# Performance work log

Measured on AMD Instinct MI355X. Metric: run time of the kernel, lower is better.

The kernel has to match this reference:

```python
import jax, jax.numpy as jnp
import numpy as np

X_SIZE = 300
H_SIZE = 128
N_CLASSES = 5
K = 3          # branching factor of the complete tree
LEVELS = 11    # tree depth (levels 0..10); N = (K**LEVELS - 1)//(K - 1) = 88573


def _build_tree():
    counts = K ** np.arange(LEVELS)
    n = int(counts.sum())
    level = np.repeat(np.arange(LEVELS), counts).astype(np.int32)
    idx = np.arange(n)
    parent = np.maximum((idx - 1) // K, 0).astype(np.int32)  # BFS numbering
    return n, parent, level


def setup_inputs() -> dict:
    key = jax.random.key(0)
    ks = jax.random.split(key, 8)
    n, parent, level = _build_tree()
    s = 0.05  # weight init scale
    return {
        "x": jax.random.normal(ks[0], (n, X_SIZE), jnp.float32),
        "mask": jax.random.randint(ks[1], (n,), 0, 2).astype(bool),
        "W_iou": jax.random.normal(ks[2], (X_SIZE, 3 * H_SIZE), jnp.float32) * s,
        "b_iou": jnp.zeros((3 * H_SIZE,), jnp.float32),
        "W_f": jax.random.normal(ks[3], (X_SIZE, H_SIZE), jnp.float32) * s,
        "b_f": jnp.zeros((H_SIZE,), jnp.float32),
        "U_iou": jax.random.normal(ks[4], (H_SIZE, 3 * H_SIZE), jnp.float32) * s,
        "U_f": jax.random.normal(ks[5], (H_SIZE, H_SIZE), jnp.float32) * s,
        "W_out": jax.random.normal(ks[6], (H_SIZE, N_CLASSES), jnp.float32) * s,
        "b_out": jnp.zeros((N_CLASSES,), jnp.float32),
        "parent": jnp.asarray(parent),
        "level": jnp.asarray(level),
        "n_levels": LEVELS,
    }


def reference(x, mask, W_iou, b_iou, W_f, b_f, U_iou, U_f, W_out, b_out,
              parent, level, n_levels):
    n = x.shape[0]
    h_size = U_f.shape[0]
    m = mask.astype(x.dtype)[:, None]                  # [N,1]
    embeds = x * m                                     # input_module = identity
    iou_in = (embeds @ W_iou + b_iou) * m              # [N,3H]
    f_in = (embeds @ W_f + b_f) * m                    # [N,H]

    h = jnp.zeros((n, h_size), x.dtype)
    c = jnp.zeros((n, h_size), x.dtype)
    par = parent[1:]                                   # edge child->parent, children are nodes 1..N-1

    # bottom-up topological propagation, one level at a time (child-sum cell)
    for lvl in range(n_levels - 1, -1, -1):
        h_ch = h[1:]                                   # children hidden states
        f = jax.nn.sigmoid(f_in[par] + h_ch @ U_f)     # per-edge forget gate
        h_sum = jax.ops.segment_sum(h_ch, par, num_segments=n)
        fc_sum = jax.ops.segment_sum(f * c[1:], par, num_segments=n)
        iou = iou_in + h_sum @ U_iou
        i, o, u = jnp.split(iou, 3, axis=-1)
        i, o, u = jax.nn.sigmoid(i), jax.nn.sigmoid(o), jnp.tanh(u)
        c_new = i * u + fc_sum
        h_new = o * jnp.tanh(c_new)
        at = (level == lvl)[:, None]
        h = jnp.where(at, h_new, h)
        c = jnp.where(at, c_new, c)

    return h @ W_out + b_out                           # output_module: Linear(H, 5)
```

## Files before the change

kernel.cpp:

```cpp
#include <hip/hip_runtime.h>
#include <hip/hip_bf16.h>
#include <math.h>

#define H 128
#define XS 300
#define NCLS 5
#define KPAD 320
#define NXCD 8

typedef __attribute__((ext_vector_type(8))) short short8;
typedef __attribute__((ext_vector_type(4))) float f32x4;

static __device__ inline unsigned short f2bf(float f) {
    __hip_bfloat16 h = __float2bfloat16(f);
    return *reinterpret_cast<unsigned short*>(&h);
}
static __device__ inline float bf2f(unsigned short u) {
    unsigned int x = ((unsigned int)u) << 16;
    return __builtin_bit_cast(float, x);
}
static __device__ inline float sigm(float v) { return 1.f / (1.f + __expf(-v)); }

__global__ void mask_conv_kernel(const void* __restrict__ mask_raw,
                                 float* __restrict__ m, int n) {
    const unsigned int* w = (const unsigned int*)mask_raw;
    bool is_bytes = false;
#pragma unroll
    for (int i = 0; i < 16; i++) is_bytes |= (w[i] > 1u);
    int idx = blockIdx.x * blockDim.x + threadIdx.x;
    if (idx >= n) return;
    float mv;
    if (is_bytes) mv = ((const unsigned char*)mask_raw)[idx] ? 1.f : 0.f;
    else          mv = ((const int*)mask_raw)[idx] ? 1.f : 0.f;
    m[idx] = mv;
}

__global__ void wconv_kernel(const float* __restrict__ W_iou,
                             const float* __restrict__ W_f,
                             unsigned short* __restrict__ Wb_t) {
    int c = blockIdx.x;
    int k = threadIdx.x;
    float v = 0.f;
    if (k < XS) v = (c < 384) ? W_iou[(size_t)k * 384 + c]
                              : W_f[(size_t)k * 128 + (c - 384)];
    Wb_t[(size_t)c * KPAD + k] = f2bf(v);
}

__global__ void uconv_kernel(const float* __restrict__ U_f,
                             const float* __restrict__ U_iou,
                             unsigned short* __restrict__ Uf_hi,
                             unsigned short* __restrict__ Uf_lo,
                             unsigned short* __restrict__ Uiou_hi,
                             unsigned short* __restrict__ Uiou_lo) {
    int c = blockIdx.x;
    int k = threadIdx.x;
    if (c < 128) {
        float v = U_f[(size_t)k * 128 + c];
        unsigned short hi = f2bf(v);
        Uf_hi[(size_t)c * 128 + k] = hi;
        Uf_lo[(size_t)c * 128 + k] = f2bf(v - bf2f(hi));
    } else {
        int cc = c - 128;
        float v = U_iou[(size_t)k * 384 + cc];
        unsigned short hi = f2bf(v);
        Uiou_hi[(size_t)cc * 128 + k] = hi;
        Uiou_lo[(size_t)cc * 128 + k] = f2bf(v - bf2f(hi));
    }
}

__global__ __launch_bounds__(256) void gemm_in_mfma(
    const float* __restrict__ x, const float* __restrict__ m,
    const unsigned short* __restrict__ Wb_t,
    const float* __restrict__ b_iou, const float* __restrict__ b_f,
    float* __restrict__ iou_in, float* __restrict__ f_in, int n)
{
    __shared__ __align__(16) unsigned short Asld[128][72];
    __shared__ __align__(16) unsigned short Bsld[128][72];

    int bid = blockIdx.x;
    int nwg = gridDim.x;
    int q = nwg / NXCD, r = nwg % NXCD;
    int xcd = bid % NXCD, slot = bid / NXCD;
    int nid = (xcd < r) ? (xcd * (q + 1) + slot)
                        : (r * (q + 1) + (xcd - r) * q + slot);
    int bn = nid & 3;
    int bm = nid >> 2;

    int t    = threadIdx.x;
    int lane = t & 63;
    int wid  = t >> 6;
    int wr = wid >> 1, wc = wid & 1;

    int r0 = bm * 128;
    int c0 = bn * 128;

    f32x4 acc[4][4];
#pragma unroll
    for (int i = 0; i < 4; i++)
#pragma unroll
        for (int j = 0; j < 4; j++) acc[i][j] = (f32x4)0.f;

    for (int k0 = 0; k0 < KPAD; k0 += 64) {
        {
            int rr = t >> 4;
            int kq = (t & 15) << 2;
            int kg = k0 + kq;
#pragma unroll
            for (int p = 0; p < 8; p++) {
                int row  = r0 + rr + p * 16;
                int rowc = row < n ? row : n - 1;
                float4 v;
                if (kg + 4 <= XS) v = *(const float4*)&x[(size_t)rowc * XS + kg];
                else              v = make_float4(0.f, 0.f, 0.f, 0.f);
                ushort4 b4;
                b4.x = f2bf(v.x); b4.y = f2bf(v.y);
                b4.z = f2bf(v.z); b4.w = f2bf(v.w);
                *(ushort4*)&Asld[rr + p * 16][kq] = b4;
            }
        }
        {
            int rr  = t >> 3;
            int kq8 = (t & 7) << 3;
#pragma unroll
            for (int p = 0; p < 4; p++) {
                int col = c0 + rr + p * 32;
                uint4 v = *(const uint4*)&Wb_t[(size_t)col * KPAD + k0 + kq8];
                *(uint4*)&Bsld[rr + p * 32][kq8] = v;
            }
        }
        __syncthreads();

#pragma unroll
        for (int ks = 0; ks < 2; ks++) {
            int kc = ks * 32 + (lane >> 4) * 8;
            short8 af[4], bf[4];
#pragma unroll
            for (int mi = 0; mi < 4; mi++)
                af[mi] = *(const short8*)&Asld[wr * 64 + mi * 16 + (lane & 15)][kc];
#pragma unroll
            for (int ni = 0; ni < 4; ni++)
                bf[ni] = *(const short8*)&Bsld[wc * 64 + ni * 16 + (lane & 15)][kc];
#pragma unroll
            for (int mi = 0; mi < 4; mi++)
#pragma unroll
                for (int ni = 0; ni < 4; ni++)
                    acc[mi][ni] = __builtin_amdgcn_mfma_f32_16x16x32_bf16(
                        af[mi], bf[ni], acc[mi][ni], 0, 0, 0);
        }
        __syncthreads();
    }

    const float* bias;
    float* outp;
    int ldw, colbase;
    if (bn < 3) { bias = b_iou; outp = iou_in; ldw = 384; colbase = bn * 128; }
    else        { bias = b_f;   outp = f_in;   ldw = 128; colbase = 0; }

    float bias_v[4];
#pragma unroll
    for (int ni = 0; ni < 4; ni++)
        bias_v[ni] = bias[colbase + wc * 64 + ni * 16 + (lane & 15)];

#pragma unroll
    for (int mi = 0; mi < 4; mi++) {
#pragma unroll
        for (int j = 0; j < 4; j++) {
            int row = r0 + wr * 64 + mi * 16 + (lane >> 4) * 4 + j;
            if (row >= n) continue;
            float mv = m[row];
#pragma unroll
            for (int ni = 0; ni < 4; ni++) {
                int col = colbase + wc * 64 + ni * 16 + (lane & 15);
                outp[(size_t)row * ldw + col] = mv * (acc[mi][ni][j] + bias_v[ni]);
            }
        }
    }
}

__global__ void leaf_kernel(const float* __restrict__ iou_in,
                            unsigned short* __restrict__ h_hi,
                            unsigned short* __restrict__ h_lo,
                            float* __restrict__ c,
                            int start, int count)
{
    int idx = blockIdx.x * blockDim.x + threadIdx.x;
    int total = count * 32;
    if (idx >= total) return;
    int v = start + (idx >> 5);
    int d = (idx & 31) * 4;
    const float* row = iou_in + (size_t)v * 384;
    float4 iv = *(const float4*)&row[d];
    float4 ov = *(const float4*)&row[128 + d];
    float4 uv = *(const float4*)&row[256 + d];
    float cv[4], hv[4];
    float ivv[4] = {iv.x, iv.y, iv.z, iv.w};
    float ovv[4] = {ov.x, ov.y, ov.z, ov.w};
    float uvv[4] = {uv.x, uv.y, uv.z, uv.w};
#pragma unroll
    for (int e = 0; e < 4; e++) {
        float ig = sigm(ivv[e]), og = sigm(ovv[e]), ug = tanhf(uvv[e]);
        cv[e] = ig * ug;
        hv[e] = og * tanhf(cv[e]);
    }
    *(float4*)&c[(size_t)v * H + d] = make_float4(cv[0], cv[1], cv[2], cv[3]);
    ushort4 hh, hl;
    unsigned short s;
    s = f2bf(hv[0]); hh.x = s; hl.x = f2bf(hv[0] - bf2f(s));
    s = f2bf(hv[1]); hh.y = s; hl.y = f2bf(hv[1] - bf2f(s));
    s = f2bf(hv[2]); hh.z = s; hl.z = f2bf(hv[2] - bf2f(s));
    s = f2bf(hv[3]); hh.w = s; hl.w = f2bf(hv[3] - bf2f(s));
    *(ushort4*)&h_hi[(size_t)v * H + d] = hh;
    *(ushort4*)&h_lo[(size_t)v * H + d] = hl;
}

__global__ __launch_bounds__(256) void level_gemm_f(
    const unsigned short* __restrict__ h_hi, const unsigned short* __restrict__ h_lo,
    const float* __restrict__ c, float* fbuf,
    const unsigned short* __restrict__ Uf_hi, const unsigned short* __restrict__ Uf_lo,
    int P0, int NP)
{
    __shared__ __align__(16) unsigned short Ah[64][136];
    __shared__ __align__(16) unsigned short Al[64][136];

    int C0 = 3 * P0 + 1;
    int M3 = 3 * NP;
    int r0 = blockIdx.x * 64;
    int t = threadIdx.x;

    {
        int tr = t >> 2;
        int tk = (t & 3) * 32;
        bool vr = (r0 + tr) < M3;
        size_t gb = (size_t)(C0 + r0 + tr) * H + tk;
        uint4 z = {0, 0, 0, 0};
#pragma unroll
        for (int kk = 0; kk < 4; kk++) {
            uint4 vh = vr ? *(const uint4*)&h_hi[gb + kk * 8] : z;
            uint4 vl = vr ? *(const uint4*)&h_lo[gb + kk * 8] : z;
            *(uint4*)&Ah[tr][tk + kk * 8] = vh;
            *(uint4*)&Al[tr][tk + kk * 8] = vl;
        }
    }
    __syncthreads();

    int lane = t & 63;
    int wid  = t >> 6;
    int nb = wid * 32;

    f32x4 acc[4][2];
#pragma unroll
    for (int mi = 0; mi < 4; mi++)
#pragma unroll
        for (int nf = 0; nf < 2; nf++) acc[mi][nf] = (f32x4)0.f;

#pragma unroll
    for (int ks = 0; ks < 4; ks++) {
        int kb = ks * 32 + (lane >> 4) * 8;
        short8 ah[4], al[4], bh[2], bl[2];
#pragma unroll
        for (int mi = 0; mi < 4; mi++) {
            ah[mi] = *(const short8*)&Ah[mi * 16 + (lane & 15)][kb];
            al[mi] = *(const short8*)&Al[mi * 16 + (lane & 15)][kb];
        }
#pragma unroll
        for (int nf = 0; nf < 2; nf++) {
            int bc = nb + nf * 16 + (lane & 15);
            bh[nf] = *(const short8*)&Uf_hi[(size_t)bc * 128 + kb];
            bl[nf] = *(const short8*)&Uf_lo[(size_t)bc * 128 + kb];
        }
#pragma unroll
        for (int mi = 0; mi < 4; mi++)
#pragma unroll
            for (int nf = 0; nf < 2; nf++) {
                acc[mi][nf] = __builtin_amdgcn_mfma_f32_16x16x32_bf16(ah[mi], bh[nf], acc[mi][nf], 0, 0, 0);
                acc[mi][nf] = __builtin_amdgcn_mfma_f32_16x16x32_bf16(ah[mi], bl[nf], acc[mi][nf], 0, 0, 0);
                acc[mi][nf] = __builtin_amdgcn_mfma_f32_16x16x32_bf16(al[mi], bh[nf], acc[mi][nf], 0, 0, 0);
            }
    }

#pragma unroll
    for (int mi = 0; mi < 4; mi++)
#pragma unroll
        for (int j = 0; j < 4; j++) {
            int rl = r0 + mi * 16 + (lane >> 4) * 4 + j;
            if (rl >= M3) continue;
            int gc = C0 + rl;
            int gp = P0 + rl / 3;
#pragma unroll
            for (int nf = 0; nf < 2; nf++) {
                int col = nb + nf * 16 + (lane & 15);
                float s = acc[mi][nf][j] + fbuf[(size_t)gp * H + col];
                fbuf[(size_t)gc * H + col] = sigm(s) * c[(size_t)gc * H + col];
            }
        }
}

__global__ __launch_bounds__(256) void level_gemm_iou(
    const float* __restrict__ iou_in, float* fbuf,
    const unsigned short* __restrict__ Uiou_hi, const unsigned short* __restrict__ Uiou_lo,
    unsigned short* h_hi, unsigned short* h_lo, float* c,
    int P0, int NP)
{
    __shared__ __align__(16) unsigned short Ah[64][136];
    __shared__ __align__(16) unsigned short Al[64][136];

    int C0 = 3 * P0 + 1;
    int r0 = blockIdx.x * 64;
    int t = threadIdx.x;

    {
        int tr = t >> 2;
        int tk = (t & 3) * 32;
        int p = r0 + tr;
        bool vr = p < NP;
#pragma unroll
        for (int kk = 0; kk < 4; kk++) {
            int k8 = tk + kk * 8;
            float hs[8];
#pragma unroll
            for (int e = 0; e < 8; e++) hs[e] = 0.f;
            if (vr) {
#pragma unroll
                for (int j = 0; j < 3; j++) {
                    size_t cb = (size_t)(C0 + 3 * p + j) * H + k8;
                    short8 hh = *(const short8*)&h_hi[cb];
                    short8 hl = *(const short8*)&h_lo[cb];
#pragma unroll
                    for (int e = 0; e < 8; e++)
                        hs[e] += bf2f((unsigned short)hh[e]) + bf2f((unsigned short)hl[e]);
                }
            }
            short8 sh, sl;
#pragma unroll
            for (int e = 0; e < 8; e++) {
                unsigned short hi = f2bf(hs[e]);
                sh[e] = (short)hi;
                sl[e] = (short)f2bf(hs[e] - bf2f(hi));
            }
            *(short8*)&Ah[tr][k8] = sh;
            *(short8*)&Al[tr][k8] = sl;
        }
    }
    __syncthreads();

    int lane = t & 63;
    int wid  = t >> 6;
    int d0 = wid * 32;

    f32x4 acc[4][2][3];
#pragma unroll
    for (int mi = 0; mi < 4; mi++)
#pragma unroll
        for (int cn = 0; cn < 2; cn++)
#pragma unroll
            for (int pl = 0; pl < 3; pl++) acc[mi][cn][pl] = (f32x4)0.f;

#pragma unroll
    for (int ks = 0; ks < 4; ks++) {
        int kb = ks * 32 + (lane >> 4) * 8;
        short8 ah[4], al[4];
#pragma unroll
        for (int mi = 0; mi < 4; mi++) {
            ah[mi] = *(const short8*)&Ah[mi * 16 + (lane & 15)][kb];
            al[mi] = *(const short8*)&Al[mi * 16 + (lane & 15)][kb];
        }
        short8 bh[2][3], bl[2][3];
#pragma unroll
        for (int cn = 0; cn < 2; cn++)
#pragma unroll
            for (int pl = 0; pl < 3; pl++) {
                int bc = d0 + cn * 16 + pl * 128 + (lane & 15);
                bh[cn][pl] = *(const short8*)&Uiou_hi[(size_t)bc * 128 + kb];
                bl[cn][pl] = *(const short8*)&Uiou_lo[(size_t)bc * 128 + kb];
            }
#pragma unroll
        for (int mi = 0; mi < 4; mi++)
#pragma unroll
            for (int cn = 0; cn < 2; cn++)
#pragma unroll
                for (int pl = 0; pl < 3; pl++) {
                    acc[mi][cn][pl] = __builtin_amdgcn_mfma_f32_16x16x32_bf16(ah[mi], bh[cn][pl], acc[mi][cn][pl], 0, 0, 0);
                    acc[mi][cn][pl] = __builtin_amdgcn_mfma_f32_16x16x32_bf16(ah[mi], bl[cn][pl], acc[mi][cn][pl], 0, 0, 0);
                    acc[mi][cn][pl] = __builtin_amdgcn_mfma_f32_16x16x32_bf16(al[mi], bh[cn][pl], acc[mi][cn][pl], 0, 0, 0);
                }
    }

#pragma unroll
    for (int mi = 0; mi < 4; mi++)
#pragma unroll
        for (int j = 0; j < 4; j++) {
            int rl = r0 + mi * 16 + (lane >> 4) * 4 + j;
            if (rl >= NP) continue;
            int v = P0 + rl;
            int cb = C0 + 3 * rl;
#pragma unroll
            for (int cn = 0; cn < 2; cn++) {
                int col = d0 + cn * 16 + (lane & 15);
                size_t iob = (size_t)v * 384 + col;
                float iv = sigm(iou_in[iob]       + acc[mi][cn][0][j]);
                float ov = sigm(iou_in[iob + 128] + acc[mi][cn][1][j]);
                float uv = tanhf(iou_in[iob + 256] + acc[mi][cn][2][j]);
                float fcs = fbuf[(size_t)cb * H + col]
                          + fbuf[(size_t)(cb + 1) * H + col]
                          + fbuf[(size_t)(cb + 2) * H + col];
                float cv = iv * uv + fcs;
                float hv = ov * tanhf(cv);
                c[(size_t)v * H + col] = cv;
                unsigned short hi = f2bf(hv);
                h_hi[(size_t)v * H + col] = hi;
                h_lo[(size_t)v * H + col] = f2bf(hv - bf2f(hi));
            }
        }
}

__global__ __launch_bounds__(256) void out_kernel(
    const unsigned short* __restrict__ h_hi, const unsigned short* __restrict__ h_lo,
    const float* __restrict__ W_out, const float* __restrict__ b_out,
    float* __restrict__ out, int n)
{
    int wave = (blockIdx.x * blockDim.x + threadIdx.x) >> 6;
    int lane = threadIdx.x & 63;
    if (wave >= n) return;
    size_t hb = (size_t)wave * H;
    float h0 = bf2f(h_hi[hb + lane]) + bf2f(h_lo[hb + lane]);
    float h1 = bf2f(h_hi[hb + lane + 64]) + bf2f(h_lo[hb + lane + 64]);
    float a[NCLS];
#pragma unroll
    for (int j = 0; j < NCLS; j++)
        a[j] = h0 * W_out[lane * NCLS + j] + h1 * W_out[(lane + 64) * NCLS + j];
#pragma unroll
    for (int off = 32; off > 0; off >>= 1)
#pragma unroll
        for (int j = 0; j < NCLS; j++)
            a[j] += __shfl_down(a[j], off, 64);
    if (lane == 0) {
#pragma unroll
        for (int j = 0; j < NCLS; j++)
            out[(size_t)wave * NCLS + j] = a[j] + b_out[j];
    }
}

extern "C" void kernel_launch(void* const* d_in, const int* in_sizes, int n_in,
                              void* d_out, int out_size, void* d_ws, size_t ws_size,
                              hipStream_t stream) {
    const float* x     = (const float*)d_in[0];
    const void*  mask  = d_in[1];
    const float* W_iou = (const float*)d_in[2];
    const float* b_iou = (const float*)d_in[3];
    const float* W_f   = (const float*)d_in[4];
    const float* b_f   = (const float*)d_in[5];
    const float* U_iou = (const float*)d_in[6];
    const float* U_f   = (const float*)d_in[7];
    const float* W_out = (const float*)d_in[8];
    const float* b_out = (const float*)d_in[9];
    float* out = (float*)d_out;

    int n = in_sizes[1];
    size_t nn = (size_t)n;
    size_t mpad = (nn + 7) & ~(size_t)7;

    float* ws     = (float*)d_ws;
    float* iou_in = ws;
    float* f_in   = iou_in + nn * 384;
    float* cbuf   = f_in   + nn * 128;
    float* mbuf   = cbuf   + nn * 128;
    unsigned short* h_hi = (unsigned short*)(mbuf + mpad);
    unsigned short* h_lo = h_hi + nn * 128;
    unsigned short* Uf_hi   = h_lo + nn * 128;
    unsigned short* Uf_lo   = Uf_hi + 128 * 128;
    unsigned short* Uiou_hi = Uf_lo + 128 * 128;
    unsigned short* Uiou_lo = Uiou_hi + 384 * 128;
    unsigned short* Wb_t = h_hi;

    int pow3[11];
    pow3[0] = 1;
    for (int i = 1; i < 11; i++) pow3[i] = pow3[i - 1] * 3;

    mask_conv_kernel<<<(n + 255) / 256, 256, 0, stream>>>(mask, mbuf, n);
    wconv_kernel<<<512, KPAD, 0, stream>>>(W_iou, W_f, Wb_t);
    uconv_kernel<<<512, 128, 0, stream>>>(U_f, U_iou, Uf_hi, Uf_lo, Uiou_hi, Uiou_lo);

    {
        int nwg = 4 * ((n + 127) / 128);
        gemm_in_mfma<<<nwg, 256, 0, stream>>>(x, mbuf, Wb_t, b_iou, b_f,
                                              iou_in, f_in, n);
    }

    {
        int start = (pow3[10] - 1) / 2;
        int count = pow3[10];
        int total = count * 32;
        leaf_kernel<<<(total + 255) / 256, 256, 0, stream>>>(iou_in, h_hi, h_lo,
                                                             cbuf, start, count);
    }

    for (int lvl = 9; lvl >= 0; --lvl) {
        int NP = pow3[lvl];
        int P0 = (pow3[lvl] - 1) / 2;
        int g1 = (3 * NP + 63) / 64;
        level_gemm_f<<<g1, 256, 0, stream>>>(h_hi, h_lo, cbuf, f_in,
                                             Uf_hi, Uf_lo, P0, NP);
        int g2 = (NP + 63) / 64;
        level_gemm_iou<<<g2, 256, 0, stream>>>(iou_in, f_in, Uiou_hi, Uiou_lo,
                                               h_hi, h_lo, cbuf, P0, NP);
    }

    {
        int blocks = (n + 3) / 4;
        out_kernel<<<blocks, 256, 0, stream>>>(h_hi, h_lo, W_out, b_out, out, n);
    }
}
```

Baseline: 793.2 us.

## Fuse per-level forget and iou GEMMs, store h as single bf16, pre-convert x

Merges the two per-level kernels into one block that loads child hidden states once into shared memory. Inside that block it computes the forget gates and reduces f*c into parents with shared-memory atomics, then forms h_sum and runs the iou GEMM. Hidden states are now stored as a single bf16 array instead of a hi/lo pair, which drops the lo-correction MFMAs and halves h traffic at the cost of precision. A new pre-pass converts x to padded bf16 so the input GEMM can do plain 16-byte loads, which adds an extra kernel and an extra pass over x.

```diff
diff --git a/kernel.cpp b/kernel.cpp
--- a/kernel.cpp
+++ b/kernel.cpp
@@ -33,6 +33,21 @@
     if (is_bytes) mv = ((const unsigned char*)mask_raw)[idx] ? 1.f : 0.f;
     else          mv = ((const int*)mask_raw)[idx] ? 1.f : 0.f;
     m[idx] = mv;
+}
+
+__global__ void xconv_kernel(const float* __restrict__ x,
+                             unsigned short* __restrict__ xb, int n) {
+    int idx = blockIdx.x * blockDim.x + threadIdx.x;
+    int total = n * (KPAD / 2);
+    if (idx >= total) return;
+    int row = idx / (KPAD / 2);
+    int kp  = (idx - row * (KPAD / 2)) * 2;
+    ushort2 o;
+    if (kp < XS) {
+        float2 v = *(const float2*)&x[(size_t)row * XS + kp];
+        o.x = f2bf(v.x); o.y = f2bf(v.y);
+    } else { o.x = 0; o.y = 0; }
+    *(ushort2*)&xb[(size_t)row * KPAD + kp] = o;
 }
 
 __global__ void wconv_kernel(const float* __restrict__ W_iou,
@@ -69,7 +84,7 @@
 }
 
 __global__ __launch_bounds__(256) void gemm_in_mfma(
-    const float* __restrict__ x, const float* __restrict__ m,
+    const unsigned short* __restrict__ xb, const float* __restrict__ m,
     const unsigned short* __restrict__ Wb_t,
     const float* __restrict__ b_iou, const float* __restrict__ b_f,
     float* __restrict__ iou_in, float* __restrict__ f_in, int n)
@@ -102,20 +117,15 @@
 
     for (int k0 = 0; k0 < KPAD; k0 += 64) {
         {
-            int rr = t >> 4;
-            int kq = (t & 15) << 2;
-            int kg = k0 + kq;
-#pragma unroll
-            for (int p = 0; p < 8; p++) {
-                int row  = r0 + rr + p * 16;
-                int rowc = row < n ? row : n - 1;
-                float4 v;
-                if (kg + 4 <= XS) v = *(const float4*)&x[(size_t)rowc * XS + kg];
-                else              v = make_float4(0.f, 0.f, 0.f, 0.f);
-                ushort4 b4;
-                b4.x = f2bf(v.x); b4.y = f2bf(v.y);
-                b4.z = f2bf(v.z); b4.w = f2bf(v.w);
-                *(ushort4*)&Asld[rr + p * 16][kq] = b4;
+            int rr = t >> 1;
+            int half = t & 1;
+            int row = r0 + rr;
+            int rowc = row < n ? row : n - 1;
+            size_t gb = (size_t)rowc * KPAD + k0 + half * 32;
+#pragma unroll
+            for (int p = 0; p < 4; p++) {
+                uint4 v = *(const uint4*)&xb[gb + p * 8];
+                *(uint4*)&Asld[rr][half * 32 + p * 8] = v;
             }
         }
         {
@@ -178,8 +188,7 @@
 }
 
 __global__ void leaf_kernel(const float* __restrict__ iou_in,
-                            unsigned short* __restrict__ h_hi,
-                            unsigned short* __restrict__ h_lo,
+                            unsigned short* __restrict__ h_bf,
                             float* __restrict__ c,
                             int start, int count)
 {
@@ -192,10 +201,10 @@
     float4 iv = *(const float4*)&row[d];
     float4 ov = *(const float4*)&row[128 + d];
     float4 uv = *(const float4*)&row[256 + d];
-    float cv[4], hv[4];
     float ivv[4] = {iv.x, iv.y, iv.z, iv.w};
     float ovv[4] = {ov.x, ov.y, ov.z, ov.w};
     float uvv[4] = {uv.x, uv.y, uv.z, uv.w};
+    float cv[4], hv[4];
 #pragma unroll
     for (int e = 0; e < 4; e++) {
         float ig = sigm(ivv[e]), og = sigm(ovv[e]), ug = tanhf(uvv[e]);
@@ -203,218 +212,157 @@
         hv[e] = og * tanhf(cv[e]);
     }
     *(float4*)&c[(size_t)v * H + d] = make_float4(cv[0], cv[1], cv[2], cv[3]);
-    ushort4 hh, hl;
-    unsigned short s;
-    s = f2bf(hv[0]); hh.x = s; hl.x = f2bf(hv[0] - bf2f(s));
-    s = f2bf(hv[1]); hh.y = s; hl.y = f2bf(hv[1] - bf2f(s));
-    s = f2bf(hv[2]); hh.z = s; hl.z = f2bf(hv[2] - bf2f(s));
-    s = f2bf(hv[3]); hh.w = s; hl.w = f2bf(hv[3] - bf2f(s));
-    *(ushort4*)&h_hi[(size_t)v * H + d] = hh;
-    *(ushort4*)&h_lo[(size_t)v * H + d] = hl;
-}
-
-__global__ __launch_bounds__(256) void level_gemm_f(
-    const unsigned short* __restrict__ h_hi, const unsigned short* __restrict__ h_lo,
-    const float* __restrict__ c, float* fbuf,
+    ushort4 hh;
+    hh.x = f2bf(hv[0]); hh.y = f2bf(hv[1]);
+    hh.z = f2bf(hv[2]); hh.w = f2bf(hv[3]);
+    *(ushort4*)&h_bf[(size_t)v * H + d] = hh;
+}
+
+__global__ __launch_bounds__(128) void level_fused(
+    const float* __restrict__ iou_in, const float* __restrict__ f_in,
     const unsigned short* __restrict__ Uf_hi, const unsigned short* __restrict__ Uf_lo,
+    const unsigned short* __restrict__ Uiou_hi, const unsigned short* __restrict__ Uiou_lo,
+    unsigned short* __restrict__ h_bf, float* __restrict__ c,
     int P0, int NP)
 {
-    __shared__ __align__(16) unsigned short Ah[64][136];
-    __shared__ __align__(16) unsigned short Al[64][136];
-
+    __shared__ __align__(16) unsigned short chH[96][136];
+    __shared__ float fcs[32][128];
+
+    int t = threadIdx.x;
     int C0 = 3 * P0 + 1;
+    int pBase = blockIdx.x * 32;
+    int chBase = 3 * pBase;
     int M3 = 3 * NP;
-    int r0 = blockIdx.x * 64;
-    int t = threadIdx.x;
-
-    {
-        int tr = t >> 2;
-        int tk = (t & 3) * 32;
-        bool vr = (r0 + tr) < M3;
-        size_t gb = (size_t)(C0 + r0 + tr) * H + tk;
-        uint4 z = {0, 0, 0, 0};
-#pragma unroll
-        for (int kk = 0; kk < 4; kk++) {
-            uint4 vh = vr ? *(const uint4*)&h_hi[gb + kk * 8] : z;
-            uint4 vl = vr ? *(const uint4*)&h_lo[gb + kk * 8] : z;
-            *(uint4*)&Ah[tr][tk + kk * 8] = vh;
-            *(uint4*)&Al[tr][tk + kk * 8] = vl;
-        }
+
+#pragma unroll
+    for (int qq = 0; qq < 12; qq++) {
+        int i = t + qq * 128;
+        int row = i >> 4, c16 = i & 15;
+        int gr = chBase + row;
+        int src = (gr < M3) ? (C0 + gr) : C0;
+        uint4 v = *(const uint4*)&h_bf[(size_t)src * H + c16 * 8];
+        *(uint4*)&chH[row][c16 * 8] = v;
+    }
+#pragma unroll
+    for (int qq = 0; qq < 32; qq++) {
+        int i = t + qq * 128;
+        fcs[i >> 7][i & 127] = 0.f;
     }
     __syncthreads();
 
-    int lane = t & 63;
-    int wid  = t >> 6;
-    int nb = wid * 32;
-
-    f32x4 acc[4][2];
-#pragma unroll
-    for (int mi = 0; mi < 4; mi++)
-#pragma unroll
-        for (int nf = 0; nf < 2; nf++) acc[mi][nf] = (f32x4)0.f;
+    int lane = t & 63, w = t >> 6;
+    int l16 = lane & 15, l4 = lane >> 4;
+
+    f32x4 facc[3][8];
+#pragma unroll
+    for (int mi = 0; mi < 3; mi++)
+#pragma unroll
+        for (int nf = 0; nf < 8; nf++) facc[mi][nf] = (f32x4)0.f;
 
 #pragma unroll
     for (int ks = 0; ks < 4; ks++) {
-        int kb = ks * 32 + (lane >> 4) * 8;
-        short8 ah[4], al[4], bh[2], bl[2];
-#pragma unroll
-        for (int mi = 0; mi < 4; mi++) {
-            ah[mi] = *(const short8*)&Ah[mi * 16 + (lane & 15)][kb];
-            al[mi] = *(const short8*)&Al[mi * 16 + (lane & 15)][kb];
-        }
-#pragma unroll
-        for (int nf = 0; nf < 2; nf++) {
-            int bc = nb + nf * 16 + (lane & 15);
-            bh[nf] = *(const short8*)&Uf_hi[(size_t)bc * 128 + kb];
-            bl[nf] = *(const short8*)&Uf_lo[(size_t)bc * 128 + kb];
-        }
-#pragma unroll
-        for (int mi = 0; mi < 4; mi++)
-#pragma unroll
-            for (int nf = 0; nf < 2; nf++) {
-                acc[mi][nf] = __builtin_amdgcn_mfma_f32_16x16x32_bf16(ah[mi], bh[nf], acc[mi][nf], 0, 0, 0);
-                acc[mi][nf] = __builtin_amdgcn_mfma_f32_16x16x32_bf16(ah[mi], bl[nf], acc[mi][nf], 0, 0, 0);
-                acc[mi][nf] = __builtin_amdgcn_mfma_f32_16x16x32_bf16(al[mi], bh[nf], acc[mi][nf], 0, 0, 0);
+        int kb = ks * 32 + l4 * 8;
+        short8 ah[3];
+#pragma unroll
+        for (int mi = 0; mi < 3; mi++)
+            ah[mi] = *(const short8*)&chH[w * 48 + mi * 16 + l16][kb];
+#pragma unroll
+        for (int nf = 0; nf < 8; nf++) {
+            int bc = nf * 16 + l16;
+            short8 bh = *(const short8*)&Uf_hi[(size_t)bc * 128 + kb];
+            short8 bl = *(const short8*)&Uf_lo[(size_t)bc * 128 + kb];
+#pragma unroll
+            for (int mi = 0; mi < 3; mi++) {
+                facc[mi][nf] = __builtin_amdgcn_mfma_f32_16x16x32_bf16(ah[mi], bh, facc[mi][nf], 0, 0, 0);
+                facc[mi][nf] = __builtin_amdgcn_mfma_f32_16x16x32_bf16(ah[mi], bl, facc[mi][nf], 0, 0, 0);
             }
-    }
-
-#pragma unroll
-    for (int mi = 0; mi < 4; mi++)
+        }
+    }
+#pragma unroll
+    for (int mi = 0; mi < 3; mi++)
 #pragma unroll
         for (int j = 0; j < 4; j++) {
-            int rl = r0 + mi * 16 + (lane >> 4) * 4 + j;
-            if (rl >= M3) continue;
-            int gc = C0 + rl;
-            int gp = P0 + rl / 3;
-#pragma unroll
-            for (int nf = 0; nf < 2; nf++) {
-                int col = nb + nf * 16 + (lane & 15);
-                float s = acc[mi][nf][j] + fbuf[(size_t)gp * H + col];
-                fbuf[(size_t)gc * H + col] = sigm(s) * c[(size_t)gc * H + col];
+            int lrow = w * 48 + mi * 16 + l4 * 4 + j;
+            int gr = chBase + lrow;
+            if (gr >= M3) continue;
+            int gchild = C0 + gr;
+            int lpar = lrow / 3;
+            int gpar = P0 + pBase + lpar;
+#pragma unroll
+            for (int nf = 0; nf < 8; nf++) {
+                int col = nf * 16 + l16;
+                float s = facc[mi][nf][j] + f_in[(size_t)gpar * H + col];
+                float fc = sigm(s) * c[(size_t)gchild * H + col];
+                atomicAdd(&fcs[lpar][col], fc);
             }
         }
-}
-
-__global__ __launch_bounds__(256) void level_gemm_iou(
-    const float* __restrict__ iou_in, float* fbuf,
-    const unsigned short* __restrict__ Uiou_hi, const unsigned short* __restrict__ Uiou_lo,
-    unsigned short* h_hi, unsigned short* h_lo, float* c,
-    int P0, int NP)
-{
-    __shared__ __align__(16) unsigned short Ah[64][136];
-    __shared__ __align__(16) unsigned short Al[64][136];
-
-    int C0 = 3 * P0 + 1;
-    int r0 = blockIdx.x * 64;
-    int t = threadIdx.x;
-
-    {
-        int tr = t >> 2;
-        int tk = (t & 3) * 32;
-        int p = r0 + tr;
-        bool vr = p < NP;
-#pragma unroll
-        for (int kk = 0; kk < 4; kk++) {
-            int k8 = tk + kk * 8;
-            float hs[8];
-#pragma unroll
-            for (int e = 0; e < 8; e++) hs[e] = 0.f;
-            if (vr) {
-#pragma unroll
-                for (int j = 0; j < 3; j++) {
-                    size_t cb = (size_t)(C0 + 3 * p + j) * H + k8;
-                    short8 hh = *(const short8*)&h_hi[cb];
-                    short8 hl = *(const short8*)&h_lo[cb];
-#pragma unroll
-                    for (int e = 0; e < 8; e++)
-                        hs[e] += bf2f((unsigned short)hh[e]) + bf2f((unsigned short)hl[e]);
-                }
-            }
-            short8 sh, sl;
-#pragma unroll
-            for (int e = 0; e < 8; e++) {
-                unsigned short hi = f2bf(hs[e]);
-                sh[e] = (short)hi;
-                sl[e] = (short)f2bf(hs[e] - bf2f(hi));
-            }
-            *(short8*)&Ah[tr][k8] = sh;
-            *(short8*)&Al[tr][k8] = sl;
-        }
-    }
     __syncthreads();
 
-    int lane = t & 63;
-    int wid  = t >> 6;
-    int d0 = wid * 32;
-
-    f32x4 acc[4][2][3];
-#pragma unroll
-    for (int mi = 0; mi < 4; mi++)
-#pragma unroll
-        for (int cn = 0; cn < 2; cn++)
-#pragma unroll
-            for (int pl = 0; pl < 3; pl++) acc[mi][cn][pl] = (f32x4)0.f;
+    short8 sreg[4];
+#pragma unroll
+    for (int qq = 0; qq < 4; qq++) {
+        int i = t + qq * 128;
+        int p = i >> 4, c16 = i & 15;
+        float hs[8];
+#pragma unroll
+        for (int e = 0; e < 8; e++) hs[e] = 0.f;
+#pragma unroll
+        for (int ch = 0; ch < 3; ch++) {
+            short8 hv = *(const short8*)&chH[3 * p + ch][c16 * 8];
+#pragma unroll
+            for (int e = 0; e < 8; e++) hs[e] += bf2f((unsigned short)hv[e]);
+        }
+#pragma unroll
+        for (int e = 0; e < 8; e++) sreg[qq][e] = (short)f2bf(hs[e]);
+    }
+    __syncthreads();
+#pragma unroll
+    for (int qq = 0; qq < 4; qq++) {
+        int i = t + qq * 128;
+        *(short8*)&chH[i >> 4][(i & 15) * 8] = sreg[qq];
+    }
+    __syncthreads();
+
+    f32x4 acc2[24];
+#pragma unroll
+    for (int nf = 0; nf < 24; nf++) acc2[nf] = (f32x4)0.f;
 
 #pragma unroll
     for (int ks = 0; ks < 4; ks++) {
-        int kb = ks * 32 + (lane >> 4) * 8;
-        short8 ah[4], al[4];
-#pragma unroll
-        for (int mi = 0; mi < 4; mi++) {
-            ah[mi] = *(const short8*)&Ah[mi * 16 + (lane & 15)][kb];
-            al[mi] = *(const short8*)&Al[mi * 16 + (lane & 15)][kb];
-        }
-        short8 bh[2][3], bl[2][3];
-#pragma unroll
-        for (int cn = 0; cn < 2; cn++)
-#pragma unroll
-            for (int pl = 0; pl < 3; pl++) {
-                int bc = d0 + cn * 16 + pl * 128 + (lane & 15);
-                bh[cn][pl] = *(const short8*)&Uiou_hi[(size_t)bc * 128 + kb];
-                bl[cn][pl] = *(const short8*)&Uiou_lo[(size_t)bc * 128 + kb];
-            }
-#pragma unroll
-        for (int mi = 0; mi < 4; mi++)
-#pragma unroll
-            for (int cn = 0; cn < 2; cn++)
-#pragma unroll
-                for (int pl = 0; pl < 3; pl++) {
-                    acc[mi][cn][pl] = __builtin_amdgcn_mfma_f32_16x16x32_bf16(ah[mi], bh[cn][pl], acc[mi][cn][pl], 0, 0, 0);
-                    acc[mi][cn][pl] = __builtin_amdgcn_mfma_f32_16x16x32_bf16(ah[mi], bl[cn][pl], acc[mi][cn][pl], 0, 0, 0);
-                    acc[mi][cn][pl] = __builtin_amdgcn_mfma_f32_16x16x32_bf16(al[mi], bh[cn][pl], acc[mi][cn][pl], 0, 0, 0);
-                }
-    }
-
-#pragma unroll
-    for (int mi = 0; mi < 4; mi++)
-#pragma unroll
-        for (int j = 0; j < 4; j++) {
-            int rl = r0 + mi * 16 + (lane >> 4) * 4 + j;
-            if (rl >= NP) continue;
-            int v = P0 + rl;
-            int cb = C0 + 3 * rl;
-#pragma unroll
-            for (int cn = 0; cn < 2; cn++) {
-                int col = d0 + cn * 16 + (lane & 15);
-                size_t iob = (size_t)v * 384 + col;
-                float iv = sigm(iou_in[iob]       + acc[mi][cn][0][j]);
-                float ov = sigm(iou_in[iob + 128] + acc[mi][cn][1][j]);
-                float uv = tanhf(iou_in[iob + 256] + acc[mi][cn][2][j]);
-                float fcs = fbuf[(size_t)cb * H + col]
-                          + fbuf[(size_t)(cb + 1) * H + col]
-                          + fbuf[(size_t)(cb + 2) * H + col];
-                float cv = iv * uv + fcs;
-                float hv = ov * tanhf(cv);
-                c[(size_t)v * H + col] = cv;
-                unsigned short hi = f2bf(hv);
-                h_hi[(size_t)v * H + col] = hi;
-                h_lo[(size_t)v * H + col] = f2bf(hv - bf2f(hi));
-            }
-        }
+        int kb = ks * 32 + l4 * 8;
+        short8 ah = *(const short8*)&chH[w * 16 + l16][kb];
+#pragma unroll
+        for (int nf = 0; nf < 24; nf++) {
+            int bc = nf * 16 + l16;
+            short8 bh = *(const short8*)&Uiou_hi[(size_t)bc * 128 + kb];
+            short8 bl = *(const short8*)&Uiou_lo[(size_t)bc * 128 + kb];
+            acc2[nf] = __builtin_amdgcn_mfma_f32_16x16x32_bf16(ah, bh, acc2[nf], 0, 0, 0);
+            acc2[nf] = __builtin_amdgcn_mfma_f32_16x16x32_bf16(ah, bl, acc2[nf], 0, 0, 0);
+        }
+    }
+#pragma unroll
+    for (int j = 0; j < 4; j++) {
+        int lpar = w * 16 + l4 * 4 + j;
+        int prow = pBase + lpar;
+        if (prow >= NP) continue;
+        int v = P0 + prow;
+#pragma unroll
+        for (int nf8 = 0; nf8 < 8; nf8++) {
+            int col = nf8 * 16 + l16;
+            size_t iob = (size_t)v * 384 + col;
+            float iv = sigm(iou_in[iob]        + acc2[nf8][j]);
+            float ov = sigm(iou_in[iob + 128]  + acc2[nf8 + 8][j]);
+            float uv = tanhf(iou_in[iob + 256] + acc2[nf8 + 16][j]);
+            float cv = iv * uv + fcs[lpar][col];
+            float hv = ov * tanhf(cv);
+        c[(size_t)v * H + col] = cv;
+            h_bf[(size_t)v * H + col] = f2bf(hv);
+        }
+    }
 }
 
 __global__ __launch_bounds__(256) void out_kernel(
-    const unsigned short* __restrict__ h_hi, const unsigned short* __restrict__ h_lo,
+    const unsigned short* __restrict__ h_bf,
     const float* __restrict__ W_out, const float* __restrict__ b_out,
     float* __restrict__ out, int n)
 {
@@ -422,8 +370,8 @@
     int lane = threadIdx.x & 63;
     if (wave >= n) return;
     size_t hb = (size_t)wave * H;
-    float h0 = bf2f(h_hi[hb + lane]) + bf2f(h_lo[hb + lane]);
-    float h1 = bf2f(h_hi[hb + lane + 64]) + bf2f(h_lo[hb + lane + 64]);
+    float h0 = bf2f(h_bf[hb + lane]);
+    float h1 = bf2f(h_bf[hb + lane + 64]);
     float a[NCLS];
 #pragma unroll
     for (int j = 0; j < NCLS; j++)
@@ -462,27 +410,31 @@
     float* ws     = (float*)d_ws;
     float* iou_in = ws;
     float* f_in   = iou_in + nn * 384;
-    float* cbuf   = f_in   + nn * 128;
-    float* mbuf   = cbuf   + nn * 128;
-    unsigned short* h_hi = (unsigned short*)(mbuf + mpad);
-    unsigned short* h_lo = h_hi + nn * 128;
-    unsigned short* Uf_hi   = h_lo + nn * 128;
+    float* mbuf   = f_in   + nn * 128;
+    float* cbuf   = mbuf   + mpad;
+    unsigned short* h_bf = (unsigned short*)(cbuf + nn * 128);
+    unsigned short* Uf_hi   = h_bf + nn * 128;
     unsigned short* Uf_lo   = Uf_hi + 128 * 128;
     unsigned short* Uiou_hi = Uf_lo + 128 * 128;
     unsigned short* Uiou_lo = Uiou_hi + 384 * 128;
-    unsigned short* Wb_t = h_hi;
+    unsigned short* xb   = (unsigned short*)cbuf;
+    unsigned short* Wb_t = xb + nn * KPAD;
 
     int pow3[11];
     pow3[0] = 1;
     for (int i = 1; i < 11; i++) pow3[i] = pow3[i - 1] * 3;
 
     mask_conv_kernel<<<(n + 255) / 256, 256, 0, stream>>>(mask, mbuf, n);
+    {
+        int total = n * (KPAD / 2);
+        xconv_kernel<<<(total + 255) / 256, 256, 0, stream>>>(x, xb, n);
+    }
     wconv_kernel<<<512, KPAD, 0, stream>>>(W_iou, W_f, Wb_t);
     uconv_kernel<<<512, 128, 0, stream>>>(U_f, U_iou, Uf_hi, Uf_lo, Uiou_hi, Uiou_lo);
 
     {
         int nwg = 4 * ((n + 127) / 128);
-        gemm_in_mfma<<<nwg, 256, 0, stream>>>(x, mbuf, Wb_t, b_iou, b_f,
+        gemm_in_mfma<<<nwg, 256, 0, stream>>>(xb, mbuf, Wb_t, b_iou, b_f,
                                               iou_in, f_in, n);
     }
 
@@ -490,23 +442,21 @@
         int start = (pow3[10] - 1) / 2;
         int count = pow3[10];
         int total = count * 32;
-        leaf_kernel<<<(total + 255) / 256, 256, 0, stream>>>(iou_in, h_hi, h_lo,
-                                                             cbuf, start, count);
+        leaf_kernel<<<(total + 255) / 256, 256, 0, stream>>>(iou_in, h_bf, cbuf,
+                                                             start, count);
     }
 
     for (int lvl = 9; lvl >= 0; --lvl) {
         int NP = pow3[lvl];
         int P0 = (pow3[lvl] - 1) / 2;
-        int g1 = (3 * NP + 63) / 64;
-        level_gemm_f<<<g1, 256, 0, stream>>>(h_hi, h_lo, cbuf, f_in,
-                                             Uf_hi, Uf_lo, P0, NP);
-        int g2 = (NP + 63) / 64;
-        level_gemm_iou<<<g2, 256, 0, stream>>>(iou_in, f_in, Uiou_hi, Uiou_lo,
-                                               h_hi, h_lo, cbuf, P0, NP);
+        int blocks = (NP + 31) / 32;
+        level_fused<<<blocks, 128, 0, stream>>>(iou_in, f_in,
+                                                Uf_hi, Uf_lo, Uiou_hi, Uiou_lo,
+                                                h_bf, cbuf, P0, NP);
     }
 
     {
         int blocks = (n + 3) / 4;
-        out_kernel<<<blocks, 256, 0, stream>>>(h_hi, h_lo, W_out, b_out, out, n);
-    }
-}
+        out_kernel<<<blocks, 256, 0, stream>>>(h_bf, W_out, b_out, out, n);
+    }
+}
```

After: 872.6 us. +10.0%, slower.
